# Optimization experiments

Measured on AMD Instinct MI355X. Metric: run time of the kernel, lower is better.

## Reference

```python
import jax, jax.numpy as jnp
import numpy as np

SIZE = 4096


def fast_hadamard_transform(x, normalize=True):
    """Walsh-Hadamard transform along last dim via log2(n) butterfly stages."""
    orig_shape = x.shape
    n = orig_shape[-1]
    h = 1
    while h < n:
        # view as (..., n//(2h), 2, h) and butterfly the pair axis
        x = x.reshape(orig_shape[:-1] + (n // (2 * h), 2, h))
        a = x[..., 0, :]
        b = x[..., 1, :]
        x = jnp.stack([a + b, a - b], axis=-2).reshape(orig_shape)
        h *= 2
    if normalize:
        x = x * (1.0 / np.sqrt(n)).astype(x.dtype)
    return x


def setup_inputs() -> dict:
    key = jax.random.key(0)
    kx, ks, kb = jax.random.split(key, 3)
    x = jax.random.normal(kx, (4, 4096, SIZE), dtype=jnp.float32)
    # adaptive_init: scale ~ N(1.0, 0.1), shift ~ N(0.0, 0.01)
    scale = 1.0 + 0.1 * jax.random.normal(ks, (SIZE,), dtype=jnp.float32)
    shift = 0.01 * jax.random.normal(kb, (SIZE,), dtype=jnp.float32)
    return {"x": x, "scale": scale, "shift": shift}


def reference(x, scale, shift):
    x_h = fast_hadamard_transform(x, normalize=True)
    return scale * x_h + shift
```

## Files before the change

### kernel.cpp

```cpp
#include <hip/hip_runtime.h>


#define ROW 4096
#define NT 256
#define RPB 8
#define S2 277
#define SI1 17

__device__ __forceinline__ void wht16(float v[16]) {
#pragma unroll
  for (int h = 1; h < 16; h <<= 1) {
#pragma unroll
    for (int i = 0; i < 16; ++i) {
      if ((i & h) == 0) {
        float a = v[i], b = v[i | h];
        v[i] = a + b;
        v[i | h] = a - b;
      }
    }
  }
}

__device__ __forceinline__ void glld16(const float* g, float* l) {
  __builtin_amdgcn_global_load_lds(
      (const __attribute__((address_space(1))) void*)g,
      (__attribute__((address_space(3))) void*)l, 16, 0, 0);
}

#define WAIT_VM(N)                                      \
  asm volatile("s_waitcnt vmcnt(" #N ")" ::: "memory"); \
  __builtin_amdgcn_sched_barrier(0)
#define WAIT_LGKM                                     \
  asm volatile("s_waitcnt lgkmcnt(0)" ::: "memory"); \
  __builtin_amdgcn_sched_barrier(0)
#define BAR asm volatile("s_barrier" ::: "memory")

__global__ __launch_bounds__(NT, 4) void AdaptiveHadamardTransform_kernel(
    const float* __restrict__ x, const float* __restrict__ scale,
    const float* __restrict__ shift, float* __restrict__ out) {
  __shared__ float stage[ROW];
  __shared__ float work[16 * S2];

  const int t = threadIdx.x;
  const int wid = t >> 6, lane = t & 63;
  const long long row0 = (long long)blockIdx.x * RPB;

  float4 sc[4], sh[4];
  {
    const float4* s4 = reinterpret_cast<const float4*>(scale + 16 * t);
    const float4* h4 = reinterpret_cast<const float4*>(shift + 16 * t);
#pragma unroll
    for (int q = 0; q < 4; ++q) {
      sc[q] = s4[q];
      sh[q] = h4[q];
    }
  }

  const int c1 = SI1 * (t >> 4) + (t & 15);
  const int c2 = S2 * (t >> 4) + (t & 15);
  const int c3 = S2 * (t >> 4) + SI1 * (t & 15);

  {
    const float* g = x + row0 * ROW;
#pragma unroll
    for (int q = 0; q < 4; ++q)
      glld16(g + (wid * 4 + q) * 256 + lane * 4, &stage[(wid * 4 + q) * 256]);
  }
  WAIT_VM(0);
  BAR;

  float v[16];
  const float norm = 0.015625f;

  for (int r = 0; r < RPB; ++r) {
    const long long base = (row0 + r) * ROW;

    if (r) {
      WAIT_VM(4);
      BAR;
    }

#pragma unroll
    for (int k = 0; k < 16; ++k) v[k] = stage[t + 256 * k];
    wht16(v);
#pragma unroll
    for (int k = 0; k < 16; ++k) work[S2 * k + c1] = v[k];
    WAIT_LGKM;
    BAR;

    if (r + 1 < RPB) {
      const float* g = x + base + ROW;
#pragma unroll
      for (int q = 0; q < 4; ++q)
        glld16(g + (wid * 4 + q) * 256 + lane * 4, &stage[(wid * 4 + q) * 256]);
    }

#pragma unroll
    for (int k = 0; k < 16; ++k) v[k] = work[c2 + SI1 * k];
    wht16(v);
#pragma unroll
    for (int k = 0; k < 16; ++k) work[c2 + SI1 * k] = v[k];
    WAIT_LGKM;
    BAR;

#pragma unroll
    for (int j = 0; j < 16; ++j) v[j] = work[c3 + j];
    wht16(v);

    float4* o4 = reinterpret_cast<float4*>(out + base + 16 * t);
#pragma unroll
    for (int q = 0; q < 4; ++q) {
      float4 o;
      o.x = fmaf(sc[q].x, v[4 * q + 0] * norm, sh[q].x);
      o.y = fmaf(sc[q].y, v[4 * q + 1] * norm, sh[q].y);
      o.z = fmaf(sc[q].z, v[4 * q + 2] * norm, sh[q].z);
      o.w = fmaf(sc[q].w, v[4 * q + 3] * norm, sh[q].w);
      o4[q] = o;
    }
  }
}

extern "C" void kernel_launch(void* const* d_in, const int* in_sizes, int n_in,
                              void* d_out, int out_size, void* d_ws, size_t ws_size,
                              hipStream_t stream) {
  const float* x = (const float*)d_in[0];
  const float* scale = (const float*)d_in[1];
  const float* shift = (const float*)d_in[2];
  float* out = (float*)d_out;

  const int rows = in_sizes[0] / ROW;
  AdaptiveHadamardTransform_kernel<<<rows / RPB, NT, 0, stream>>>(x, scale, shift, out);
}
```

Before: 450.6 us.

## Double-buffer row staging, reorder WHT passes, use nontemporal scalar stores

Result: slower. 477.0 us (+5.9%).

```diff
diff --git a/kernel.cpp b/kernel.cpp
--- a/kernel.cpp
+++ b/kernel.cpp
@@ -30,29 +30,28 @@
 #define WAIT_VM(N)                                      \
   asm volatile("s_waitcnt vmcnt(" #N ")" ::: "memory"); \
   __builtin_amdgcn_sched_barrier(0)
-#define WAIT_LGKM                                     \
+#define WAIT_LGKM                                    \
   asm volatile("s_waitcnt lgkmcnt(0)" ::: "memory"); \
   __builtin_amdgcn_sched_barrier(0)
 #define BAR asm volatile("s_barrier" ::: "memory")
 
-__global__ __launch_bounds__(NT, 4) void AdaptiveHadamardTransform_kernel(
+__global__ __launch_bounds__(NT, 3) void AdaptiveHadamardTransform_kernel(
     const float* __restrict__ x, const float* __restrict__ scale,
     const float* __restrict__ shift, float* __restrict__ out) {
-  __shared__ float stage[ROW];
+  __shared__ float stage[2][ROW];
   __shared__ float work[16 * S2];
 
   const int t = threadIdx.x;
   const int wid = t >> 6, lane = t & 63;
   const long long row0 = (long long)blockIdx.x * RPB;
 
-  float4 sc[4], sh[4];
+  float sc[16], sh[16];
   {
-    const float4* s4 = reinterpret_cast<const float4*>(scale + 16 * t);
-    const float4* h4 = reinterpret_cast<const float4*>(shift + 16 * t);
+    const int eb = 256 * (t >> 4) + (t & 15);
 #pragma unroll
-    for (int q = 0; q < 4; ++q) {
-      sc[q] = s4[q];
-      sh[q] = h4[q];
+    for (int k = 0; k < 16; ++k) {
+      sc[k] = scale[eb + 16 * k];
+      sh[k] = shift[eb + 16 * k];
     }
   }
 
@@ -64,7 +63,7 @@
     const float* g = x + row0 * ROW;
 #pragma unroll
     for (int q = 0; q < 4; ++q)
-      glld16(g + (wid * 4 + q) * 256 + lane * 4, &stage[(wid * 4 + q) * 256]);
+      glld16(g + (wid * 4 + q) * 256 + lane * 4, &stage[0][(wid * 4 + q) * 256]);
   }
   WAIT_VM(0);
   BAR;
@@ -72,50 +71,53 @@
   float v[16];
   const float norm = 0.015625f;
 
+#pragma unroll
   for (int r = 0; r < RPB; ++r) {
     const long long base = (row0 + r) * ROW;
 
+    if (r + 1 < RPB) {
+      const float* g = x + base + ROW;
+      float* dst = stage[(r + 1) & 1];
+#pragma unroll
+      for (int q = 0; q < 4; ++q)
+        glld16(g + (wid * 4 + q) * 256 + lane * 4, dst + (wid * 4 + q) * 256);
+    }
+
     if (r) {
-      WAIT_VM(4);
+      if (r + 1 < RPB) {
+        WAIT_VM(20);
+      } else {
+        WAIT_VM(16);
+      }
       BAR;
     }
 
+    const float* sbuf = stage[r & 1];
 #pragma unroll
-    for (int k = 0; k < 16; ++k) v[k] = stage[t + 256 * k];
+    for (int k = 0; k < 16; ++k) v[k] = sbuf[t + 256 * k];
     wht16(v);
 #pragma unroll
     for (int k = 0; k < 16; ++k) work[S2 * k + c1] = v[k];
     WAIT_LGKM;
     BAR;
 
-    if (r + 1 < RPB) {
-      const float* g = x + base + ROW;
 #pragma unroll
-      for (int q = 0; q < 4; ++q)
-        glld16(g + (wid * 4 + q) * 256 + lane * 4, &stage[(wid * 4 + q) * 256]);
-    }
+    for (int k = 0; k < 16; ++k) v[k] = work[c3 + k];
+    wht16(v);
+#pragma unroll
+    for (int k = 0; k < 16; ++k) work[c3 + k] = v[k];
+    WAIT_LGKM;
+    BAR;
 
 #pragma unroll
     for (int k = 0; k < 16; ++k) v[k] = work[c2 + SI1 * k];
     wht16(v);
+
+    float* orow = out + base + 256 * (t >> 4) + (t & 15);
 #pragma unroll
-    for (int k = 0; k < 16; ++k) work[c2 + SI1 * k] = v[k];
-    WAIT_LGKM;
-    BAR;
-
-#pragma unroll
-    for (int j = 0; j < 16; ++j) v[j] = work[c3 + j];
-    wht16(v);
-
-    float4* o4 = reinterpret_cast<float4*>(out + base + 16 * t);
-#pragma unroll
-    for (int q = 0; q < 4; ++q) {
-      float4 o;
-      o.x = fmaf(sc[q].x, v[4 * q + 0] * norm, sh[q].x);
-      o.y = fmaf(sc[q].y, v[4 * q + 1] * norm, sh[q].y);
-      o.z = fmaf(sc[q].z, v[4 * q + 2] * norm, sh[q].z);
-      o.w = fmaf(sc[q].w, v[4 * q + 3] * norm, sh[q].w);
-      o4[q] = o;
+    for (int k = 0; k < 16; ++k) {
+      const float o = fmaf(sc[k], v[k] * norm, sh[k]);
+      __builtin_nontemporal_store(o, orow + 16 * k);
     }
   }
 }
```
